# Performance work log

Measured on AMD Instinct MI355X. Metric: run time of the kernel, lower is better.

## Reference

```python
import jax, jax.numpy as jnp
import numpy as np

TEMP = 0.5
EPS = 1e-8  # torch CosineSimilarity eps


def setup_inputs() -> dict:
    key = jax.random.key(0)
    k1, k2 = jax.random.split(key)
    B, D = 4096, 256
    return {
        "features1": jax.random.normal(k1, (B, D), dtype=jnp.float32),
        "features2": jax.random.normal(k2, (B, D), dtype=jnp.float32),
    }


def reference(features1, features2):
    B = features1.shape[0]
    f = jnp.concatenate([features1, features2], axis=0)  # [2B, D]
    # cosine similarity matrix via norms + GEMM (same math as broadcasted cos)
    n = jnp.sqrt(jnp.sum(f * f, axis=-1))  # [2B]
    dots = f @ f.T  # [2B, 2B]
    logits = dots / jnp.maximum(n[:, None] * n[None, :], EPS) / TEMP
    # labels = cat([arange(B), arange(B)]) -- faithful to the source module
    labels = jnp.concatenate([jnp.arange(B), jnp.arange(B)], axis=0)  # [2B]
    lse = jax.nn.logsumexp(logits, axis=1)  # [2B]
    picked = logits[jnp.arange(2 * B), labels]  # [2B]
    return jnp.mean(lse - picked)
```

## Files before the change

kernel.cpp:

```cpp
#include <hip/hip_runtime.h>
#include <hip/hip_bf16.h>
#include <math.h>


#define B_ROWS 4096
#define D_DIM  256
#define N_ROWS 8192
#define BM     128
#define BN     64
#define NCHUNK 8
#define CHUNK_COLS (N_ROWS / NCHUNK)
#define TILES_PER_CHUNK (CHUNK_COLS / BN)

typedef __attribute__((ext_vector_type(8))) short short8;
typedef __attribute__((ext_vector_type(4))) float f32x4;

__device__ __forceinline__ float bf2f(unsigned short u) {
  union { unsigned int i; float f; } p; p.i = ((unsigned int)u) << 16; return p.f;
}

__global__ __launch_bounds__(256) void nt_normalize(const float* __restrict__ f1,
                                                    const float* __restrict__ f2,
                                                    unsigned short* __restrict__ G) {
  const int row  = blockIdx.x * 4 + (threadIdx.x >> 6);
  const int lane = threadIdx.x & 63;
  const float* src = (row < B_ROWS) ? (f1 + (size_t)row * D_DIM)
                                    : (f2 + (size_t)(row - B_ROWS) * D_DIM);
  float4 v = reinterpret_cast<const float4*>(src)[lane];
  float ss = v.x * v.x + v.y * v.y + v.z * v.z + v.w * v.w;
#pragma unroll
  for (int m = 1; m < 64; m <<= 1) ss += __shfl_xor(ss, m, 64);
  float scale = 1.41421356237309515f * rsqrtf(fmaxf(ss, 1e-30f));
  union { ushort4 u; __hip_bfloat16 h[4]; } p;
  p.h[0] = __float2bfloat16(v.x * scale);
  p.h[1] = __float2bfloat16(v.y * scale);
  p.h[2] = __float2bfloat16(v.z * scale);
  p.h[3] = __float2bfloat16(v.w * scale);
  reinterpret_cast<ushort4*>(G + (size_t)row * D_DIM)[lane] = p.u;
}

__global__ __launch_bounds__(256) void nt_picked(const unsigned short* __restrict__ G,
                                                 float* __restrict__ picked) {
  const int row  = blockIdx.x * 4 + (threadIdx.x >> 6);
  const int lane = threadIdx.x & 63;
  const int lbl  = (row < B_ROWS) ? row : (row - B_ROWS);
  ushort4 a = reinterpret_cast<const ushort4*>(G + (size_t)row * D_DIM)[lane];
  ushort4 b = reinterpret_cast<const ushort4*>(G + (size_t)lbl * D_DIM)[lane];
  float s = bf2f(a.x) * bf2f(b.x) + bf2f(a.y) * bf2f(b.y) +
            bf2f(a.z) * bf2f(b.z) + bf2f(a.w) * bf2f(b.w);
#pragma unroll
  for (int m = 1; m < 64; m <<= 1) s += __shfl_xor(s, m, 64);
  if (lane == 0) picked[row] = s;
}

__device__ __forceinline__ void stage_lds(const char* gsrc_base, char* lds_base,
                                          int rounds, int tid) {
  const int lane = tid & 63, wid = tid >> 6;
  for (int r = 0; r < rounds; ++r) {
    const int o  = r * 4096 + wid * 1024 + lane * 16;
    const int so = o ^ (((o >> 9) & 7) << 4);
    __builtin_amdgcn_global_load_lds(
        (const __attribute__((address_space(1))) void*)(gsrc_base + so),
        (__attribute__((address_space(3))) void*)(lds_base + r * 4096 + wid * 1024),
        16, 0, 0);
  }
}

__global__ __launch_bounds__(256, 2) void nt_gemm_rowsum(
    const unsigned short* __restrict__ G,
    float* __restrict__ partial)
{
  const int bid   = blockIdx.x;
  const int rb    = bid / NCHUNK;
  const int chunk = bid % NCHUNK;
  const int tid   = threadIdx.x;
  const int lane  = tid & 63;
  const int wid   = tid >> 6;
  const int wr    = wid >> 1;
  const int wc    = wid & 1;

  __shared__ short8 lds8[4096];
  char* ldsb = reinterpret_cast<char*>(lds8);
  const char* gbytes = reinterpret_cast<const char*>(G);

  stage_lds(gbytes + (size_t)rb * BM * D_DIM * 2, ldsb, 16, tid);
  __syncthreads();

  short8 afrag[4][8];
  {
    const int r0 = wr * 64;
#pragma unroll
    for (int m = 0; m < 4; ++m) {
      const int row = r0 + m * 16 + (lane & 15);
      const int sw  = (row & 7) << 4;
#pragma unroll
      for (int ks = 0; ks < 8; ++ks) {
        const int off = (row * 512 + ks * 64 + ((lane >> 4) << 4)) ^ sw;
        afrag[m][ks] = *reinterpret_cast<const short8*>(ldsb + off);
      }
    }
  }
  __syncthreads();

  float rowsum[16];
#pragma unroll
  for (int i = 0; i < 16; ++i) rowsum[i] = 0.f;

  const size_t colbase = (size_t)chunk * CHUNK_COLS;

  stage_lds(gbytes + (colbase + 0) * 512, ldsb, 8, tid);
  __syncthreads();

  for (int t = 0; t < TILES_PER_CHUNK; ++t) {
    const int cur = t & 1;
    if (t + 1 < TILES_PER_CHUNK)
      stage_lds(gbytes + (colbase + (size_t)(t + 1) * BN) * 512,
                ldsb + ((t + 1) & 1) * 32768, 8, tid);

    char* bbuf = ldsb + cur * 32768;
    f32x4 acc[4][2] = {};
#pragma unroll
    for (int ks = 0; ks < 8; ++ks) {
      short8 bfrag[2];
#pragma unroll
      for (int n = 0; n < 2; ++n) {
        const int brow = wc * 32 + n * 16 + (lane & 15);
        const int off  = (brow * 512 + ks * 64 + ((lane >> 4) << 4)) ^ ((brow & 7) << 4);
        bfrag[n] = *reinterpret_cast<const short8*>(bbuf + off);
      }
#pragma unroll
      for (int m = 0; m < 4; ++m)
#pragma unroll
        for (int n = 0; n < 2; ++n)
          acc[m][n] = __builtin_amdgcn_mfma_f32_16x16x32_bf16(
              afrag[m][ks], bfrag[n], acc[m][n], 0, 0, 0);
    }
#pragma unroll
    for (int m = 0; m < 4; ++m)
#pragma unroll
      for (int n = 0; n < 2; ++n)
#pragma unroll
        for (int j = 0; j < 4; ++j)
          rowsum[m * 4 + j] += __expf(acc[m][n][j]);
    __syncthreads();
  }

#pragma unroll
  for (int i = 0; i < 16; ++i) {
    float s = rowsum[i];
    s += __shfl_xor(s, 1, 64);
    s += __shfl_xor(s, 2, 64);
    s += __shfl_xor(s, 4, 64);
    s += __shfl_xor(s, 8, 64);
    rowsum[i] = s;
  }
  __syncthreads();
  float* red = reinterpret_cast<float*>(ldsb);
  if ((lane & 15) == 0) {
    const int g = lane >> 4;
#pragma unroll
    for (int i = 0; i < 16; ++i) {
      const int m = i >> 2, j = i & 3;
      red[wc * 128 + wr * 64 + m * 16 + g * 4 + j] = rowsum[i];
    }
  }
  __syncthreads();
  if (tid < 128) {
    const float s = red[tid] + red[128 + tid];
    partial[(size_t)chunk * N_ROWS + (size_t)rb * BM + tid] = s;
  }
}

__global__ __launch_bounds__(1024) void nt_finalize(const float* __restrict__ partial,
                                                    const float* __restrict__ picked,
                                                    float* __restrict__ out) {
  __shared__ float red[16];
  const int tid = threadIdx.x;
  float local = 0.f;
  for (int r = tid; r < N_ROWS; r += 1024) {
    float s = 0.f;
#pragma unroll
    for (int c = 0; c < NCHUNK; ++c) s += partial[(size_t)c * N_ROWS + r];
    local += __logf(s) - picked[r];
  }
#pragma unroll
  for (int m = 1; m < 64; m <<= 1) local += __shfl_xor(local, m, 64);
  if ((tid & 63) == 0) red[tid >> 6] = local;
  __syncthreads();
  if (tid < 64) {
    float v = (tid < 16) ? red[tid] : 0.f;
#pragma unroll
    for (int m = 1; m < 16; m <<= 1) v += __shfl_xor(v, m, 64);
    if (tid == 0) out[0] = v / (float)N_ROWS;
  }
}

extern "C" void kernel_launch(void* const* d_in, const int* in_sizes, int n_in,
                              void* d_out, int out_size, void* d_ws, size_t ws_size,
                              hipStream_t stream) {
  const float* f1 = (const float*)d_in[0];
  const float* f2 = (const float*)d_in[1];
  float* out = (float*)d_out;

  char* ws = (char*)d_ws;
  unsigned short* G = (unsigned short*)ws;
  float* partial = (float*)(ws + (size_t)4 * 1024 * 1024);
  float* picked  = (float*)(ws + (size_t)4 * 1024 * 1024 + 256 * 1024);

  hipLaunchKernelGGL(nt_normalize, dim3(N_ROWS / 4), dim3(256), 0, stream, f1, f2, G);
  hipLaunchKernelGGL(nt_picked,    dim3(N_ROWS / 4), dim3(256), 0, stream, G, picked);
  hipLaunchKernelGGL(nt_gemm_rowsum, dim3((N_ROWS / BM) * NCHUNK), dim3(256), 0, stream,
                     G, partial);
  hipLaunchKernelGGL(nt_finalize, dim3(1), dim3(1024), 0, stream, partial, picked, out);
}
```

Baseline: 53.14 us.

## Exploit Gram matrix symmetry with lower-triangular tiles and split finalize

The similarity GEMM now computes only the lower-triangular 128x128 tiles of the symmetric Gram matrix. Each tile contributes both row sums and column sums of exp(logits), written to per-panel partial buffers, which roughly halves the MFMA and exp work. The finalize step is split into a 64-block reduction over 64 panels followed by a tiny final kernel. In exchange there are 2080 short blocks with no in-block pipelining, extra cross-lane column reductions, and a larger partial buffer to reduce.

```diff
diff --git a/kernel.cpp b/kernel.cpp
--- a/kernel.cpp
+++ b/kernel.cpp
@@ -6,11 +6,8 @@
 #define B_ROWS 4096
 #define D_DIM  256
 #define N_ROWS 8192
-#define BM     128
-#define BN     64
-#define NCHUNK 8
-#define CHUNK_COLS (N_ROWS / NCHUNK)
-#define TILES_PER_CHUNK (CHUNK_COLS / BN)
+#define NPANEL 64
+#define NTRI   2080
 
 typedef __attribute__((ext_vector_type(8))) short short8;
 typedef __attribute__((ext_vector_type(4))) float f32x4;
@@ -66,24 +63,27 @@
   }
 }
 
-__global__ __launch_bounds__(256, 2) void nt_gemm_rowsum(
+__global__ __launch_bounds__(256, 2) void nt_gemm_tri(
     const unsigned short* __restrict__ G,
     float* __restrict__ partial)
 {
-  const int bid   = blockIdx.x;
-  const int rb    = bid / NCHUNK;
-  const int chunk = bid % NCHUNK;
-  const int tid   = threadIdx.x;
-  const int lane  = tid & 63;
-  const int wid   = tid >> 6;
-  const int wr    = wid >> 1;
-  const int wc    = wid & 1;
+  int bid = (blockIdx.x & 7) * (NTRI / 8) + (blockIdx.x >> 3);
+  int rb = (int)((sqrtf(8.f * (float)bid + 1.f) - 1.f) * 0.5f);
+  while ((rb + 1) * (rb + 2) / 2 <= bid) ++rb;
+  while (rb * (rb + 1) / 2 > bid) --rb;
+  const int cb = bid - rb * (rb + 1) / 2;
+
+  const int tid  = threadIdx.x;
+  const int lane = tid & 63;
+  const int wid  = tid >> 6;
+  const int wr   = wid >> 1;
+  const int wc   = wid & 1;
 
   __shared__ short8 lds8[4096];
   char* ldsb = reinterpret_cast<char*>(lds8);
-  const char* gbytes = reinterpret_cast<const char*>(G);
-
-  stage_lds(gbytes + (size_t)rb * BM * D_DIM * 2, ldsb, 16, tid);
+  const char* gb = reinterpret_cast<const char*>(G);
+
+  stage_lds(gb + (size_t)rb * 128 * 512, ldsb, 16, tid);
   __syncthreads();
 
   short8 afrag[4][8];
@@ -102,97 +102,107 @@
   }
   __syncthreads();
 
-  float rowsum[16];
-#pragma unroll
-  for (int i = 0; i < 16; ++i) rowsum[i] = 0.f;
-
-  const size_t colbase = (size_t)chunk * CHUNK_COLS;
-
-  stage_lds(gbytes + (colbase + 0) * 512, ldsb, 8, tid);
-  __syncthreads();
-
-  for (int t = 0; t < TILES_PER_CHUNK; ++t) {
-    const int cur = t & 1;
-    if (t + 1 < TILES_PER_CHUNK)
-      stage_lds(gbytes + (colbase + (size_t)(t + 1) * BN) * 512,
-                ldsb + ((t + 1) & 1) * 32768, 8, tid);
-
-    char* bbuf = ldsb + cur * 32768;
-    f32x4 acc[4][2] = {};
-#pragma unroll
-    for (int ks = 0; ks < 8; ++ks) {
-      short8 bfrag[2];
-#pragma unroll
-      for (int n = 0; n < 2; ++n) {
-        const int brow = wc * 32 + n * 16 + (lane & 15);
-        const int off  = (brow * 512 + ks * 64 + ((lane >> 4) << 4)) ^ ((brow & 7) << 4);
-        bfrag[n] = *reinterpret_cast<const short8*>(bbuf + off);
+  stage_lds(gb + (size_t)cb * 128 * 512, ldsb, 16, tid);
+  f32x4 acc[4][4] = {};
+  __syncthreads();
+
+#pragma unroll
+  for (int ks = 0; ks < 8; ++ks) {
+    short8 bfrag[4];
+#pragma unroll
+    for (int n = 0; n < 4; ++n) {
+      const int brow = wc * 64 + n * 16 + (lane & 15);
+      const int off  = (brow * 512 + ks * 64 + ((lane >> 4) << 4)) ^ ((brow & 7) << 4);
+      bfrag[n] = *reinterpret_cast<const short8*>(ldsb + off);
+    }
+#pragma unroll
+    for (int m = 0; m < 4; ++m)
+#pragma unroll
+      for (int n = 0; n < 4; ++n)
+        acc[m][n] = __builtin_amdgcn_mfma_f32_16x16x32_bf16(
+            afrag[m][ks], bfrag[n], acc[m][n], 0, 0, 0);
+  }
+
+  float rs[16], cs[4];
+#pragma unroll
+  for (int i = 0; i < 16; ++i) rs[i] = 0.f;
+#pragma unroll
+  for (int n = 0; n < 4; ++n) cs[n] = 0.f;
+#pragma unroll
+  for (int m = 0; m < 4; ++m)
+#pragma unroll
+    for (int n = 0; n < 4; ++n)
+#pragma unroll
+      for (int j = 0; j < 4; ++j) {
+        const float e = __expf(acc[m][n][j]);
+        rs[m * 4 + j] += e;
+        cs[n] += e;
       }
 #pragma unroll
-      for (int m = 0; m < 4; ++m)
-#pragma unroll
-        for (int n = 0; n < 2; ++n)
-          acc[m][n] = __builtin_amdgcn_mfma_f32_16x16x32_bf16(
-              afrag[m][ks], bfrag[n], acc[m][n], 0, 0, 0);
-    }
-#pragma unroll
-    for (int m = 0; m < 4; ++m)
-#pragma unroll
-      for (int n = 0; n < 2; ++n)
-#pragma unroll
-        for (int j = 0; j < 4; ++j)
-          rowsum[m * 4 + j] += __expf(acc[m][n][j]);
-    __syncthreads();
-  }
-
-#pragma unroll
   for (int i = 0; i < 16; ++i) {
-    float s = rowsum[i];
+    float s = rs[i];
     s += __shfl_xor(s, 1, 64);
     s += __shfl_xor(s, 2, 64);
     s += __shfl_xor(s, 4, 64);
     s += __shfl_xor(s, 8, 64);
-    rowsum[i] = s;
-  }
-  __syncthreads();
-  float* red = reinterpret_cast<float*>(ldsb);
+    rs[i] = s;
+  }
+#pragma unroll
+  for (int n = 0; n < 4; ++n) {
+    float s = cs[n];
+    s += __shfl_xor(s, 16, 64);
+    s += __shfl_xor(s, 32, 64);
+    cs[n] = s;
+  }
+  __syncthreads();
+  float* redr = reinterpret_cast<float*>(ldsb);
+  float* redc = reinterpret_cast<float*>(ldsb + 1024);
   if ((lane & 15) == 0) {
     const int g = lane >> 4;
 #pragma unroll
-    for (int i = 0; i < 16; ++i) {
-      const int m = i >> 2, j = i & 3;
-      red[wc * 128 + wr * 64 + m * 16 + g * 4 + j] = rowsum[i];
-    }
+    for (int i = 0; i < 16; ++i)
+      redr[wc * 128 + wr * 64 + (i >> 2) * 16 + g * 4 + (i & 3)] = rs[i];
+  }
+  if ((lane >> 4) == 0) {
+#pragma unroll
+    for (int n = 0; n < 4; ++n)
+      redc[wr * 128 + wc * 64 + n * 16 + lane] = cs[n];
   }
   __syncthreads();
   if (tid < 128) {
-    const float s = red[tid] + red[128 + tid];
-    partial[(size_t)chunk * N_ROWS + (size_t)rb * BM + tid] = s;
-  }
-}
-
-__global__ __launch_bounds__(1024) void nt_finalize(const float* __restrict__ partial,
+    const float v = redr[tid] + redr[128 + tid];
+    partial[(size_t)cb * N_ROWS + (size_t)rb * 128 + tid] = v;
+  } else if (rb != cb) {
+    const int t = tid - 128;
+    const float v = redc[t] + redc[128 + t];
+    partial[(size_t)rb * N_ROWS + (size_t)cb * 128 + t] = v;
+  }
+}
+
+__global__ __launch_bounds__(128) void nt_finalize1(const float* __restrict__ partial,
                                                     const float* __restrict__ picked,
-                                                    float* __restrict__ out) {
-  __shared__ float red[16];
+                                                    float* __restrict__ loss_part) {
+  const int b = blockIdx.x, tid = threadIdx.x;
+  const int r = b * 128 + tid;
+  float s = 0.f;
+#pragma unroll
+  for (int c = 0; c < NPANEL; ++c) s += partial[(size_t)c * N_ROWS + r];
+  float local = __logf(s) - picked[r];
+#pragma unroll
+  for (int m = 1; m < 64; m <<= 1) local += __shfl_xor(local, m, 64);
+  __shared__ float red[2];
+  if ((tid & 63) == 0) red[tid >> 6] = local;
+  __syncthreads();
+  if (tid == 0) loss_part[b] = red[0] + red[1];
+}
+
+__global__ __launch_bounds__(64) void nt_finalize2(const float* __restrict__ loss_part,
+                                                   float* __restrict__ out) {
   const int tid = threadIdx.x;
-  float local = 0.f;
-  for (int r = tid; r < N_ROWS; r += 1024) {
-    float s = 0.f;
-#pragma unroll
-    for (int c = 0; c < NCHUNK; ++c) s += partial[(size_t)c * N_ROWS + r];
-    local += __logf(s) - picked[r];
-  }
-#pragma unroll
-  for (int m = 1; m < 64; m <<= 1) local += __shfl_xor(local, m, 64);
-  if ((tid & 63) == 0) red[tid >> 6] = local;
-  __syncthreads();
-  if (tid < 64) {
-    float v = (tid < 16) ? red[tid] : 0.f;
-#pragma unroll
-    for (int m = 1; m < 16; m <<= 1) v += __shfl_xor(v, m, 64);
-    if (tid == 0) out[0] = v / (float)N_ROWS;
-  }
+  float v = loss_part[tid];
+#pragma unroll
+  for (int m = 1; m < 64; m <<= 1) v += __shfl_xor(v, m, 64);
+  if (tid == 0) out[0] = v / (float)N_ROWS;
 }
 
 extern "C" void kernel_launch(void* const* d_in, const int* in_sizes, int n_in,
@@ -204,12 +214,13 @@
 
   char* ws = (char*)d_ws;
   unsigned short* G = (unsigned short*)ws;
-  float* partial = (float*)(ws + (size_t)4 * 1024 * 1024);
-  float* picked  = (float*)(ws + (size_t)4 * 1024 * 1024 + 256 * 1024);
+  float* partial   = (float*)(ws + (size_t)4 * 1024 * 1024);
+  float* picked    = (float*)(ws + (size_t)6 * 1024 * 1024);
+  float* loss_part = (float*)(ws + (size_t)6 * 1024 * 1024 + 32 * 1024);
 
   hipLaunchKernelGGL(nt_normalize, dim3(N_ROWS / 4), dim3(256), 0, stream, f1, f2, G);
   hipLaunchKernelGGL(nt_picked,    dim3(N_ROWS / 4), dim3(256), 0, stream, G, picked);
-  hipLaunchKernelGGL(nt_gemm_rowsum, dim3((N_ROWS / BM) * NCHUNK), dim3(256), 0, stream,
-                     G, partial);
-  hipLaunchKernelGGL(nt_finalize, dim3(1), dim3(1024), 0, stream, partial, picked, out);
-}
+  hipLaunchKernelGGL(nt_gemm_tri,  dim3(NTRI),       dim3(256), 0, stream, G, partial);
+  hipLaunchKernelGGL(nt_finalize1, dim3(NPANEL),     dim3(128), 0, stream, partial, picked, loss_part);
+  hipLaunchKernelGGL(nt_finalize2, dim3(1),          dim3(64),  0, stream, loss_part, out);
+}
```

Result: slower. 65.90 us (+24.0%).
